# Kernel optimization log

Measured on AMD Instinct MI355X. Metric: run time of the kernel, lower is better.

## Reference

```python
import jax, jax.numpy as jnp
import numpy as np


def _axial_mha(x, Wq, Wk, Wv, Wo, bo, n_head, axis):
    # x: (B, T, H, W, C) channels-last video features
    B, T, H, W, C = x.shape
    d = C // n_head
    scale = 1.0 / np.sqrt(d)

    def proj(w):
        return (x @ w.T).reshape(B, T, H, W, n_head, d)

    q, k, v = proj(Wq), proj(Wk), proj(Wv)
    if axis == 'w':  # attend along width
        s = jnp.einsum('bthwnd,bthvnd->bthnwv', q, k) * scale
        a = jax.nn.softmax(s, axis=-1)
        o = jnp.einsum('bthnwv,bthvnd->bthwnd', a, v)
    elif axis == 'h':  # attend along height
        s = jnp.einsum('bthwnd,btgwnd->btwnhg', q, k) * scale
        a = jax.nn.softmax(s, axis=-1)
        o = jnp.einsum('btwnhg,btgwnd->bthwnd', a, v)
    else:  # 't' attend along time
        s = jnp.einsum('bthwnd,bshwnd->bhwnts', q, k) * scale
        a = jax.nn.softmax(s, axis=-1)
        o = jnp.einsum('bhwnts,bshwnd->bthwnd', a, v)
    o = o.reshape(B, T, H, W, C)
    return o @ Wo.T + bo


def setup_inputs() -> dict:
    key = jax.random.key(0)
    ks = jax.random.split(key, 16)
    B, C, T, H, W = 4, 512, 16, 32, 32
    std = 1.0 / np.sqrt(C)
    inp = {'x': jax.random.normal(ks[0], (B, C, T, H, W), jnp.float32)}
    i = 1
    for ax in ('w', 'h', 't'):
        for nm in ('wq', 'wk', 'wv', 'wo'):
            inp[f'{nm}_{ax}'] = jax.random.normal(ks[i], (C, C), jnp.float32) * std
            i += 1
        inp[f'bo_{ax}'] = jnp.zeros((C,), jnp.float32)
    inp['n_head'] = 8
    return inp


def reference(x, wq_w, wk_w, wv_w, wo_w, bo_w,
              wq_h, wk_h, wv_h, wo_h, bo_h,
              wq_t, wk_t, wv_t, wo_t, bo_t, n_head):
    xt = jnp.moveaxis(x, 1, -1)  # (B, T, H, W, C)
    out = (_axial_mha(xt, wq_w, wk_w, wv_w, wo_w, bo_w, n_head, 'w')
           + _axial_mha(xt, wq_h, wk_h, wv_h, wo_h, bo_h, n_head, 'h')
           + _axial_mha(xt, wq_t, wk_t, wv_t, wo_t, bo_t, n_head, 't'))
    return jnp.moveaxis(out, -1, 1)  # (B, C, T, H, W)
```

## Files before the change

kernel.cpp:

```cpp
#include <hip/hip_runtime.h>

typedef float f4 __attribute__((ext_vector_type(4)));
typedef int i4 __attribute__((ext_vector_type(4)));
typedef __bf16 bf16x8 __attribute__((ext_vector_type(8)));
typedef unsigned short u16;

#define DEV static __device__ __forceinline__

DEV f4 mfma_bf16(bf16x8 a, bf16x8 b, f4 c) {
  return __builtin_amdgcn_mfma_f32_16x16x32_bf16(a, b, c, 0, 0, 0);
}

DEV bf16x8 ld_frag(const u16* p) {
  union { i4 i; bf16x8 b; } u;
  u.i = *(const i4*)p;
  return u.b;
}

DEV u16 f2bf(float f) {
  union { float f; unsigned int u; } v; v.f = f;
  return (u16)((v.u + 0x7fffu + ((v.u >> 16) & 1u)) >> 16);
}

DEV void async_cp16(const void* g, void* l) {
  __builtin_amdgcn_global_load_lds((const __attribute__((address_space(1))) void*)g,
                                   (__attribute__((address_space(3))) void*)l, 16, 0, 0);
}

__global__ __launch_bounds__(256) void k_transpose_x(const float* __restrict__ x,
                                                     u16* __restrict__ xt) {
  __shared__ float tile[32][33];
  const int b = blockIdx.z;
  const int thw0 = blockIdx.x * 32;
  const int c0 = blockIdx.y * 32;
  const int tc = threadIdx.x & 31;
  const int tr = threadIdx.x >> 5;
#pragma unroll
  for (int i = 0; i < 4; i++) {
    int c = tr + i * 8;
    tile[c][tc] = x[(long)(b * 512 + c0 + c) * 16384 + thw0 + tc];
  }
  __syncthreads();
#pragma unroll
  for (int i = 0; i < 4; i++) {
    int r = tr + i * 8;
    xt[(long)(b * 16384 + thw0 + r) * 512 + c0 + tc] = f2bf(tile[tc][r]);
  }
}

__global__ __launch_bounds__(256) void k_prep_w(
    const float* wq_w, const float* wk_w, const float* wv_w, const float* wo_w, const float* bo_w,
    const float* wq_h, const float* wk_h, const float* wv_h, const float* wo_h, const float* bo_h,
    const float* wq_t, const float* wk_t, const float* wv_t, const float* wo_t, const float* bo_t,
    u16* Wqkv, u16* WoCat, float* bo) {
  const int idx = blockIdx.x * 256 + threadIdx.x;
  if (idx < 2359296) {
    int j = idx >> 9, ci = idx & 511;
    int sel = j >> 9, co = j & 511;
    const float* s;
    switch (sel) {
      case 0: s = wq_w; break; case 1: s = wk_w; break; case 2: s = wv_w; break;
      case 3: s = wq_h; break; case 4: s = wk_h; break; case 5: s = wv_h; break;
      case 6: s = wq_t; break; case 7: s = wk_t; break; default: s = wv_t; break;
    }
    Wqkv[idx] = f2bf(s[co * 512 + ci]);
  } else if (idx < 2359296 + 786432) {
    int t = idx - 2359296;
    int c = t / 1536, j2 = t - c * 1536;
    int a = j2 >> 9, ci = j2 & 511;
    const float* s = (a == 0) ? wo_w : (a == 1) ? wo_h : wo_t;
    WoCat[t] = f2bf(s[c * 512 + ci]);
  } else if (idx < 2359296 + 786432 + 512) {
    int c = idx - (2359296 + 786432);
    bo[c] = bo_w[c] + bo_h[c] + bo_t[c];
  }
}

template <int NK, int EPI, int NT, int MT, bool MMINOR>
__global__ __launch_bounds__(512, 2) void k_gemm256(
    const u16* __restrict__ A, const u16* __restrict__ Bt,
    void* __restrict__ Co, const float* __restrict__ bias, int ldc) {
  constexpr int K = NK * 64;
  constexpr int NIT = NK / 2;
  __shared__ __attribute__((aligned(16))) u16 lds[65536];

  const int tid = threadIdx.x;
  const int lane = tid & 63, wave = tid >> 6;
  const int cl = lane & 15, q = lane >> 4;
  const int wr = wave >> 2, wc = wave & 3;

  const int bid = blockIdx.x;
  const int orig = (bid & 7) * ((NT * MT) >> 3) + (bid >> 3);
  const int my = MMINOR ? (orig % MT) : (orig / NT);
  const int nx = MMINOR ? (orig / MT) : (orig % NT);
  const long m0 = (long)my * 256;
  const long n0 = (long)nx * 256;
  const u16* Ab = A + m0 * K;
  const u16* Bb = Bt + n0 * K;

  long goff[2];
  int sdst[2];
#pragma unroll
  for (int i = 0; i < 2; i++) {
    int s = i * 512 + tid;
    int row = s >> 3;
    int c = (s & 7) ^ (row & 7);
    goff[i] = (long)row * K + c * 8;
    sdst[i] = (i * 512 + (tid & 448)) * 8;
  }

#define STG(op, h, t)                                                        \
  {                                                                          \
    const u16* gb_ = (op) ? Bb : Ab;                                         \
    u16* lb_ = lds + ((t) & 1) * 32768 + (op) * 16384 + (h) * 8192;          \
    _Pragma("unroll")                                                        \
    for (int i_ = 0; i_ < 2; i_++)                                           \
      async_cp16(gb_ + goff[i_] + (long)(h) * 128 * K + (t) * 64,            \
                 lb_ + sdst[i_]);                                            \
  }
#define BAR() __builtin_amdgcn_s_barrier()
#define WAITV(N) asm volatile("s_waitcnt vmcnt(" #N ")" ::: "memory")

  const int pk0 = (q ^ (cl & 7)) * 8;
  const int pk1 = ((q + 4) ^ (cl & 7)) * 8;
  const int arow = (wr * 128 + cl) * 64;
  const int brow = (wc * 64 + cl) * 64;

  bf16x8 a[4][2], bl[2][2], bh[2][2];

#define LD_A(bb, mh)                                                         \
  _Pragma("unroll")                                                          \
  for (int m_ = 0; m_ < 4; m_++) {                                           \
    const u16* p_ = lds + (bb) * 32768 + arow + (mh) * 4096 + m_ * 1024;     \
    a[m_][0] = ld_frag(p_ + pk0);                                            \
    a[m_][1] = ld_frag(p_ + pk1);                                            \
  }
#define LD_BL(bb)                                                            \
  _Pragma("unroll")                                                          \
  for (int n_ = 0; n_ < 2; n_++) {                                           \
    const u16* p_ = lds + (bb) * 32768 + 16384 + brow + n_ * 1024;           \
    bl[n_][0] = ld_frag(p_ + pk0);                                           \
    bl[n_][1] = ld_frag(p_ + pk1);                                           \
  }
#define LD_BH(bb)                                                            \
  _Pragma("unroll")                                                          \
  for (int n_ = 0; n_ < 2; n_++) {                                           \
    const u16* p_ = lds + (bb) * 32768 + 16384 + brow + 2048 + n_ * 1024;    \
    bh[n_][0] = ld_frag(p_ + pk0);                                           \
    bh[n_][1] = ld_frag(p_ + pk1);                                           \
  }
#define MM(mh, nh, B)                                                        \
  __builtin_amdgcn_s_setprio(1);                                             \
  _Pragma("unroll")                                                          \
  for (int m_ = 0; m_ < 4; m_++)                                             \
    _Pragma("unroll")                                                        \
    for (int n_ = 0; n_ < 2; n_++)                                           \
      _Pragma("unroll")                                                      \
      for (int ks_ = 0; ks_ < 2; ks_++)                                      \
        acc[(mh) * 4 + m_][(nh) * 2 + n_] =                                  \
            mfma_bf16(a[m_][ks_], B[n_][ks_], acc[(mh) * 4 + m_][(nh) * 2 + n_]); \
  __builtin_amdgcn_s_setprio(0);

  f4 acc[8][4];
  {
    f4 z; z[0] = z[1] = z[2] = z[3] = 0.f;
#pragma unroll
    for (int m = 0; m < 8; m++)
#pragma unroll
      for (int n = 0; n < 4; n++) acc[m][n] = z;
  }

  STG(1, 0, 0); STG(1, 1, 0); STG(0, 0, 0); STG(0, 1, 0);
  STG(1, 0, 1); STG(1, 1, 1);
  WAITV(4);
  BAR();

#define ITER_BODY(t, MORE)                                                   \
                                           \
  LD_A(0, 0); LD_BL(0); STG(0, 0, (t) + 1);                                  \
  BAR(); MM(0, 0, bl); BAR();                                                \
  LD_BH(0); STG(0, 1, (t) + 1);                                              \
  BAR(); MM(0, 1, bh); BAR();                                                \
  LD_A(0, 1); if (MORE) STG(1, 0, (t) + 2);                                  \
  BAR(); MM(1, 0, bl); BAR();                                                \
  if (MORE) { STG(1, 1, (t) + 2); WAITV(4); } else { WAITV(0); }             \
  BAR(); MM(1, 1, bh); BAR();                                                \
                                         \
  LD_A(1, 0); LD_BL(1); if (MORE) STG(0, 0, (t) + 2);                        \
  BAR(); MM(0, 0, bl); BAR();                                                \
  LD_BH(1); if (MORE) STG(0, 1, (t) + 2);                                    \
  BAR(); MM(0, 1, bh); BAR();                                                \
  LD_A(1, 1); if (MORE) STG(1, 0, (t) + 3);                                  \
  BAR(); MM(1, 0, bl); BAR();                                                \
  if (MORE) { STG(1, 1, (t) + 3); WAITV(4); } else { WAITV(0); }             \
  BAR(); MM(1, 1, bh); BAR();

#pragma unroll 1
  for (int it = 0; it < NIT - 1; ++it) {
    const int t = 2 * it;
    ITER_BODY(t, true)
  }
  {
    const int t = 2 * (NIT - 1);
    ITER_BODY(t, false)
  }
#undef ITER_BODY
#undef MM
#undef LD_A
#undef LD_BL
#undef LD_BH
#undef STG
#undef WAITV
#undef BAR

  if (EPI == 0) {
    __syncthreads();
    u16* myl = lds + wave * 4608;
    u16* CoB = (u16*)Co;
#pragma unroll
    for (int h = 0; h < 2; h++) {
      if (h) __syncthreads();
#pragma unroll
      for (int m = 0; m < 4; m++)
#pragma unroll
        for (int n = 0; n < 4; n++)
#pragma unroll
          for (int r = 0; r < 4; r++)
            myl[(m * 16 + q * 4 + r) * 72 + n * 16 + cl] = f2bf(acc[h * 4 + m][n][r]);
#pragma unroll
      for (int it = 0; it < 8; it++) {
        int lr = it * 8 + (lane >> 3);
        int lc = (lane & 7) * 8;
        i4 v = *(const i4*)(myl + lr * 72 + lc);
        *(i4*)(CoB + (m0 + wr * 128 + h * 64 + lr) * ldc + n0 + wc * 64 + lc) = v;
      }
    }
  } else {
    float* Cf = (float*)Co;
#pragma unroll
    for (int m = 0; m < 8; m++)
#pragma unroll
      for (int r = 0; r < 4; r++) {
        int c = (int)m0 + wr * 128 + m * 16 + q * 4 + r;
        float bv = bias[c];
#pragma unroll
        for (int n = 0; n < 4; n++) {
          long nn = n0 + wc * 64 + n * 16 + cl;
          long b = nn >> 14, thw = nn & 16383;
          Cf[((b * 512 + c) << 14) + thw] = acc[m][n][r] + bv;
        }
      }
  }
}

template <int L>
__global__ __launch_bounds__(64) void k_attn(
    const u16* __restrict__ QKV, u16* __restrict__ Oc,
    int inner, int istride, int ostride, int obase, int tstride) {
  constexpr int NT = L / 16;
  __shared__ __attribute__((aligned(16))) u16 sQ[2048];
  __shared__ __attribute__((aligned(16))) u16 sK[2048];
  __shared__ __attribute__((aligned(16))) u16 sVt[2560];
  __shared__ __attribute__((aligned(16))) u16 sPbuf[(L == 16) ? 1280 : 1];
  u16* sP = (L == 16) ? sPbuf : sQ;
  const int lane = threadIdx.x;
  const int cl = lane & 15, q = lane >> 4;
  const int g = blockIdx.x, head = blockIdx.y;
  const long tok0 = (long)(g / inner) * ostride + (long)(g % inner) * istride;
  const long rs = (long)tstride * 1536;
  const u16* qb = QKV + tok0 * 1536 + head * 64;
  const u16* kb = qb + 512;
  const u16* vb = qb + 1024;

  if (L == 16) {
    unsigned int* z1 = (unsigned int*)sVt;
    for (int i = lane; i < 1280; i += 64) z1[i] = 0;
    unsigned int* z2 = (unsigned int*)sPbuf;
    for (int i = lane; i < 640; i += 64) z2[i] = 0;
  }

#pragma unroll
  for (int i = 0; i < L / 8; i++) {
    int s = i * 64 + lane;
    int row = s >> 3;
    int gc = (s & 7) ^ (row & 7);
    async_cp16(qb + row * rs + gc * 8, (char*)sQ + i * 1024);
    async_cp16(kb + row * rs + gc * 8, (char*)sK + i * 1024);
  }
#pragma unroll
  for (int i = 0; i < L / 8; i++) {
    int s = i * 64 + lane;
    int row = s >> 3, c8 = s & 7;
    union { i4 v; u16 h[8]; } raw;
    raw.v = *(const i4*)(vb + row * rs + c8 * 8);
#pragma unroll
    for (int j = 0; j < 8; j++) sVt[(c8 * 8 + j) * 40 + row] = raw.h[j];
  }
  __syncthreads();

  f4 sacc[NT][NT];
  { f4 z; z[0]=z[1]=z[2]=z[3]=0.f;
    for (int a = 0; a < NT; a++) for (int b2 = 0; b2 < NT; b2++) sacc[a][b2] = z; }
#pragma unroll
  for (int kk = 0; kk < 2; kk++) {
    bf16x8 qf[NT], kf[NT];
#pragma unroll
    for (int t = 0; t < NT; t++) {
      int row = t * 16 + cl;
      int ch = (kk * 4 + q) ^ (row & 7);
      qf[t] = ld_frag(sQ + row * 64 + ch * 8);
      kf[t] = ld_frag(sK + row * 64 + ch * 8);
    }
#pragma unroll
    for (int rt = 0; rt < NT; rt++)
#pragma unroll
      for (int ct = 0; ct < NT; ct++)
        sacc[rt][ct] = mfma_bf16(qf[rt], kf[ct], sacc[rt][ct]);
  }

#pragma unroll
  for (int rt = 0; rt < NT; rt++)
#pragma unroll
    for (int ct = 0; ct < NT; ct++)
#pragma unroll
      for (int i = 0; i < 4; i++) sacc[rt][ct][i] *= 0.125f;
#pragma unroll
  for (int rt = 0; rt < NT; rt++)
#pragma unroll
    for (int i = 0; i < 4; i++) {
      float m = sacc[rt][0][i];
#pragma unroll
      for (int ct = 1; ct < NT; ct++) m = fmaxf(m, sacc[rt][ct][i]);
      for (int off = 1; off < 16; off <<= 1) m = fmaxf(m, __shfl_xor(m, off, 64));
      float ssum = 0.f;
#pragma unroll
      for (int ct = 0; ct < NT; ct++) {
        float p = __expf(sacc[rt][ct][i] - m);
        sacc[rt][ct][i] = p;
        ssum += p;
      }
      for (int off = 1; off < 16; off <<= 1) ssum += __shfl_xor(ssum, off, 64);
      float inv = 1.0f / ssum;
#pragma unroll
      for (int ct = 0; ct < NT; ct++) sacc[rt][ct][i] *= inv;
    }

#pragma unroll
  for (int rt = 0; rt < NT; rt++)
#pragma unroll
    for (int ct = 0; ct < NT; ct++)
#pragma unroll
      for (int i = 0; i < 4; i++)
        sP[(rt * 16 + q * 4 + i) * 40 + ct * 16 + cl] = f2bf(sacc[rt][ct][i]);
  __syncthreads();

  bf16x8 pf[NT], vf[4];
#pragma unroll
  for (int mt = 0; mt < NT; mt++) pf[mt] = ld_frag(sP + (mt * 16 + cl) * 40 + q * 8);
#pragma unroll
  for (int nt = 0; nt < 4; nt++) vf[nt] = ld_frag(sVt + (nt * 16 + cl) * 40 + q * 8);
  f4 oacc[NT][4];
  { f4 z; z[0]=z[1]=z[2]=z[3]=0.f;
    for (int a = 0; a < NT; a++) for (int b2 = 0; b2 < 4; b2++) oacc[a][b2] = z; }
#pragma unroll
  for (int mt = 0; mt < NT; mt++)
#pragma unroll
    for (int nt = 0; nt < 4; nt++)
      oacc[mt][nt] = mfma_bf16(pf[mt], vf[nt], oacc[mt][nt]);

#pragma unroll
  for (int mt = 0; mt < NT; mt++)
#pragma unroll
    for (int i = 0; i < 4; i++) {
      int r = mt * 16 + q * 4 + i;
      u16* dst = Oc + (tok0 + (long)r * tstride) * 1536 + obase + head * 64;
#pragma unroll
      for (int nt = 0; nt < 4; nt++) dst[nt * 16 + cl] = f2bf(oacc[mt][nt][i]);
    }
}

extern "C" void kernel_launch(void* const* d_in, const int* in_sizes, int n_in,
                              void* d_out, int out_size, void* d_ws, size_t ws_size,
                              hipStream_t stream) {
  (void)in_sizes; (void)n_in; (void)out_size; (void)ws_size;
  const float* x    = (const float*)d_in[0];
  const float* wq_w = (const float*)d_in[1];
  const float* wk_w = (const float*)d_in[2];
  const float* wv_w = (const float*)d_in[3];
  const float* wo_w = (const float*)d_in[4];
  const float* bo_w = (const float*)d_in[5];
  const float* wq_h = (const float*)d_in[6];
  const float* wk_h = (const float*)d_in[7];
  const float* wv_h = (const float*)d_in[8];
  const float* wo_h = (const float*)d_in[9];
  const float* bo_h = (const float*)d_in[10];
  const float* wq_t = (const float*)d_in[11];
  const float* wk_t = (const float*)d_in[12];
  const float* wv_t = (const float*)d_in[13];
  const float* wo_t = (const float*)d_in[14];
  const float* bo_t = (const float*)d_in[15];

  char* ws = (char*)d_ws;
  u16* xt    = (u16*)(ws);
  u16* qkv   = (u16*)(ws + 67108864L);
  u16* oc    = (u16*)(ws + 268435456L);
  u16* Wqkv  = (u16*)(ws + 469762048L);
  u16* WoCat = (u16*)(ws + 474480640L);
  float* bo  = (float*)(ws + 476053504L);

  k_transpose_x<<<dim3(512, 16, 4), 256, 0, stream>>>(x, xt);
  k_prep_w<<<dim3(12290), 256, 0, stream>>>(wq_w, wk_w, wv_w, wo_w, bo_w,
                                            wq_h, wk_h, wv_h, wo_h, bo_h,
                                            wq_t, wk_t, wv_t, wo_t, bo_t,
                                            Wqkv, WoCat, bo);
  for (int a = 0; a < 3; a++) {
    k_gemm256<8, 0, 6, 256, false><<<dim3(1536), 512, 0, stream>>>(
        xt, Wqkv + (long)a * 1536 * 512, qkv, nullptr, 1536);
    if (a == 0)
      k_attn<32><<<dim3(2048, 8), 64, 0, stream>>>(qkv, oc, 1, 0, 32, 0, 1);
    else if (a == 1)
      k_attn<32><<<dim3(2048, 8), 64, 0, stream>>>(qkv, oc, 32, 1, 1024, 512, 32);
    else
      k_attn<16><<<dim3(4096, 8), 64, 0, stream>>>(qkv, oc, 1024, 1, 16384, 1024, 1024);
  }
  k_gemm256<24, 1, 256, 2, true><<<dim3(512), 512, 0, stream>>>(
      WoCat, oc, (float*)d_out, bo, 0);
}
```

Before: 918.2 us.

## Load attention Q/K/V fragments directly from global and pack four heads per block

```diff
diff --git a/kernel.cpp b/kernel.cpp
--- a/kernel.cpp
+++ b/kernel.cpp
@@ -254,69 +254,59 @@
 }
 
 template <int L>
-__global__ __launch_bounds__(64) void k_attn(
+__global__ __launch_bounds__(256) void k_attn(
     const u16* __restrict__ QKV, u16* __restrict__ Oc,
     int inner, int istride, int ostride, int obase, int tstride) {
   constexpr int NT = L / 16;
-  __shared__ __attribute__((aligned(16))) u16 sQ[2048];
-  __shared__ __attribute__((aligned(16))) u16 sK[2048];
-  __shared__ __attribute__((aligned(16))) u16 sVt[2560];
-  __shared__ __attribute__((aligned(16))) u16 sPbuf[(L == 16) ? 1280 : 1];
-  u16* sP = (L == 16) ? sPbuf : sQ;
-  const int lane = threadIdx.x;
+  constexpr int PR = (L == 32) ? 40 : 24;
+  constexpr int PSZ = (L == 32) ? 32 * 40 : 16 * 24;
+  __shared__ __attribute__((aligned(16))) u16 sPall[4 * PSZ];
+  const int tid = threadIdx.x;
+  const int lane = tid & 63, wave = tid >> 6;
+  u16* sP = sPall + wave * PSZ;
   const int cl = lane & 15, q = lane >> 4;
-  const int g = blockIdx.x, head = blockIdx.y;
+  const int g = blockIdx.x;
+  const int head = blockIdx.y * 4 + wave;
   const long tok0 = (long)(g / inner) * ostride + (long)(g % inner) * istride;
   const long rs = (long)tstride * 1536;
   const u16* qb = QKV + tok0 * 1536 + head * 64;
   const u16* kb = qb + 512;
   const u16* vb = qb + 1024;
 
-  if (L == 16) {
-    unsigned int* z1 = (unsigned int*)sVt;
-    for (int i = lane; i < 1280; i += 64) z1[i] = 0;
-    unsigned int* z2 = (unsigned int*)sPbuf;
-    for (int i = lane; i < 640; i += 64) z2[i] = 0;
-  }
-
-#pragma unroll
-  for (int i = 0; i < L / 8; i++) {
-    int s = i * 64 + lane;
-    int row = s >> 3;
-    int gc = (s & 7) ^ (row & 7);
-    async_cp16(qb + row * rs + gc * 8, (char*)sQ + i * 1024);
-    async_cp16(kb + row * rs + gc * 8, (char*)sK + i * 1024);
-  }
-#pragma unroll
-  for (int i = 0; i < L / 8; i++) {
-    int s = i * 64 + lane;
-    int row = s >> 3, c8 = s & 7;
-    union { i4 v; u16 h[8]; } raw;
-    raw.v = *(const i4*)(vb + row * rs + c8 * 8);
-#pragma unroll
-    for (int j = 0; j < 8; j++) sVt[(c8 * 8 + j) * 40 + row] = raw.h[j];
-  }
-  __syncthreads();
+  bf16x8 qf[NT][2], kf[NT][2];
+#pragma unroll
+  for (int t = 0; t < NT; t++)
+#pragma unroll
+    for (int kk = 0; kk < 2; kk++) {
+      const long ro = (long)(t * 16 + cl) * rs + kk * 32 + q * 8;
+      qf[t][kk] = ld_frag(qb + ro);
+      kf[t][kk] = ld_frag(kb + ro);
+    }
+
+  bf16x8 vf[4];
+#pragma unroll
+  for (int nt = 0; nt < 4; nt++) {
+    union { bf16x8 v; u16 h[8]; } u;
+#pragma unroll
+    for (int j = 0; j < 8; j++) {
+      if (L == 32 || q < 2)
+        u.h[j] = vb[(long)(q * 8 + j) * rs + nt * 16 + cl];
+      else
+        u.h[j] = 0;
+    }
+    vf[nt] = u.v;
+  }
 
   f4 sacc[NT][NT];
   { f4 z; z[0]=z[1]=z[2]=z[3]=0.f;
     for (int a = 0; a < NT; a++) for (int b2 = 0; b2 < NT; b2++) sacc[a][b2] = z; }
 #pragma unroll
-  for (int kk = 0; kk < 2; kk++) {
-    bf16x8 qf[NT], kf[NT];
-#pragma unroll
-    for (int t = 0; t < NT; t++) {
-      int row = t * 16 + cl;
-      int ch = (kk * 4 + q) ^ (row & 7);
-      qf[t] = ld_frag(sQ + row * 64 + ch * 8);
-      kf[t] = ld_frag(sK + row * 64 + ch * 8);
-    }
+  for (int kk = 0; kk < 2; kk++)
 #pragma unroll
     for (int rt = 0; rt < NT; rt++)
 #pragma unroll
       for (int ct = 0; ct < NT; ct++)
-        sacc[rt][ct] = mfma_bf16(qf[rt], kf[ct], sacc[rt][ct]);
-  }
+        sacc[rt][ct] = mfma_bf16(qf[rt][kk], kf[ct][kk], sacc[rt][ct]);
 
 #pragma unroll
   for (int rt = 0; rt < NT; rt++)
@@ -351,14 +341,20 @@
     for (int ct = 0; ct < NT; ct++)
 #pragma unroll
       for (int i = 0; i < 4; i++)
-        sP[(rt * 16 + q * 4 + i) * 40 + ct * 16 + cl] = f2bf(sacc[rt][ct][i]);
-  __syncthreads();
-
-  bf16x8 pf[NT], vf[4];
-#pragma unroll
-  for (int mt = 0; mt < NT; mt++) pf[mt] = ld_frag(sP + (mt * 16 + cl) * 40 + q * 8);
-#pragma unroll
-  for (int nt = 0; nt < 4; nt++) vf[nt] = ld_frag(sVt + (nt * 16 + cl) * 40 + q * 8);
+        sP[(rt * 16 + q * 4 + i) * PR + ct * 16 + cl] = f2bf(sacc[rt][ct][i]);
+
+  bf16x8 pf[NT];
+#pragma unroll
+  for (int mt = 0; mt < NT; mt++) {
+    if (L == 32 || q < 2) {
+      pf[mt] = ld_frag(sP + (mt * 16 + cl) * PR + q * 8);
+    } else {
+      union { i4 i; bf16x8 b; } u;
+      u.i[0] = u.i[1] = u.i[2] = u.i[3] = 0;
+      pf[mt] = u.b;
+    }
+  }
+
   f4 oacc[NT][4];
   { f4 z; z[0]=z[1]=z[2]=z[3]=0.f;
     for (int a = 0; a < NT; a++) for (int b2 = 0; b2 < 4; b2++) oacc[a][b2] = z; }
@@ -417,11 +413,11 @@
     k_gemm256<8, 0, 6, 256, false><<<dim3(1536), 512, 0, stream>>>(
         xt, Wqkv + (long)a * 1536 * 512, qkv, nullptr, 1536);
     if (a == 0)
-      k_attn<32><<<dim3(2048, 8), 64, 0, stream>>>(qkv, oc, 1, 0, 32, 0, 1);
+      k_attn<32><<<dim3(2048, 2), 256, 0, stream>>>(qkv, oc, 1, 0, 32, 0, 1);
     else if (a == 1)
-      k_attn<32><<<dim3(2048, 8), 64, 0, stream>>>(qkv, oc, 32, 1, 1024, 512, 32);
+      k_attn<32><<<dim3(2048, 2), 256, 0, stream>>>(qkv, oc, 32, 1, 1024, 512, 32);
     else
-      k_attn<16><<<dim3(4096, 8), 64, 0, stream>>>(qkv, oc, 1024, 1, 16384, 1024, 1024);
+      k_attn<16><<<dim3(4096, 2), 256, 0, stream>>>(qkv, oc, 1024, 1, 16384, 1024, 1024);
   }
   k_gemm256<24, 1, 256, 2, true><<<dim3(512), 512, 0, stream>>>(
       WoCat, oc, (float*)d_out, bo, 0);
```

New measurement: 894.9 us. -2.5%, faster.
